# Performance work log

Hardware: AMD Instinct MI355X
Metric: run time of the kernel (lower is better)

The kernel has to match this reference:

```python
import jax, jax.numpy as jnp
import numpy as np

B, N = 2, 1024
DIM = 1024
DQK = 128
NUM_KEYS = 256
NUM_MEM = NUM_KEYS * NUM_KEYS
TOPK = 32
RANK = 2
HEADS = 2
DV = 512
KCONV = 5
MARGIN = 0.15
AUX_W = 0.1
MEM_LR = 10.0
RMS_EPS = 1.1920929e-07  # torch.finfo(float32).eps (RMSNorm eps=None default)
LN_EPS = 1e-5


def setup_inputs() -> dict:
    key = jax.random.key(0)
    ks = jax.random.split(key, 6)
    return {
        "tokens": jax.random.normal(ks[0], (B, N, DIM), jnp.float32),
        "rms_w": jnp.ones((DIM,), jnp.float32),
        "conv_w": jax.random.normal(ks[1], (DIM, 1, KCONV), jnp.float32) * 0.1,
        "conv_b": jnp.zeros((DIM,), jnp.float32),
        "wq": jax.random.normal(ks[2], (DQK, DIM), jnp.float32) * 0.02,
        "qln_w": jnp.ones((DQK,), jnp.float32),
        "keys": jax.random.normal(ks[3], (2, RANK, NUM_KEYS, DQK), jnp.float32) * 0.01,
        "core": jax.random.normal(ks[4], (HEADS, RANK, RANK), jnp.float32) * 0.01,
        "memories": jax.random.normal(ks[5], (NUM_MEM, DV), jnp.float32) * 0.01,
    }


def _forward(tokens, rms_w, conv_w, conv_b, wq, qln_w, keys, core, memories):
    # prenorm RMSNorm
    x = tokens * jax.lax.rsqrt(jnp.mean(tokens * tokens, -1, keepdims=True) + RMS_EPS) * rms_w
    # SVD of core; rank-1 merge vectors (first left/right singular vectors)
    u, s, vh = jnp.linalg.svd(core, full_matrices=False)
    u_vec = u[..., :, 0]   # (H, R)
    t_vec = vh[..., 0, :]  # (H, R)  == v[..., :, 0]
    aux = jnp.sum(jnp.mean(jnp.square(jax.nn.relu(s[:, 1:] - MARGIN)), -1)) * AUX_W
    # causal depthwise conv (left-pad KCONV-1)
    xc = jnp.swapaxes(x, 1, 2)  # (B, D, N)
    xc = jax.lax.conv_general_dilated(
        xc, conv_w, (1,), [(KCONV - 1, 0)],
        feature_group_count=DIM, dimension_numbers=('NCH', 'OIH', 'NCH'))
    x = jnp.swapaxes(xc + conv_b[None, :, None], 1, 2)
    # queries + LayerNorm (no bias). NOTE: original applies key_ln but then uses
    # the raw self.keys in the einsum, so key normalization is a no-op; replicated.
    q = x @ wq.T
    mu = jnp.mean(q, -1, keepdims=True)
    var = jnp.mean(jnp.square(q - mu), -1, keepdims=True)
    q = (q - mu) * jax.lax.rsqrt(var + LN_EPS) * qln_w
    # product-key scores: (2, B, N, M, R)
    sc = jnp.einsum('bnd,crmd->cbnmr', q, keys)
    row_sc, col_sc = sc[0], sc[1]  # (B, N, M, R)
    m_row = jnp.einsum('bnmr,hr->hbnm', row_sc, u_vec)
    m_col = jnp.einsum('bnmr,hr->hbnm', col_sc, t_vec)
    _, top_row = jax.lax.top_k(m_row, TOPK)  # (H, B, N, K)
    _, top_col = jax.lax.top_k(m_col, TOPK)
    # candidate flat memory indices: outer sum -> (H, B, N, K*K)
    idx = (top_row * NUM_KEYS)[..., :, None] + top_col[..., None, :]
    idx = idx.reshape(HEADS, B, N, TOPK * TOPK)
    # gather per-rank scores at the top row/col keys
    rs = jnp.broadcast_to(row_sc[None], (HEADS,) + row_sc.shape)
    cs = jnp.broadcast_to(col_sc[None], (HEADS,) + col_sc.shape)
    ri = jnp.broadcast_to(top_row[..., None], top_row.shape + (RANK,))
    ci = jnp.broadcast_to(top_col[..., None], top_col.shape + (RANK,))
    f_row = jnp.take_along_axis(rs, ri, axis=3)  # (H, B, N, K, R)
    f_col = jnp.take_along_axis(cs, ci, axis=3)
    # bilinear core combine over ranks -> (H, B, N, K, K)
    scores = jnp.einsum('hbnir,hbnjs,hrs->hbnij', f_row, f_col, core)
    scores = scores.reshape(HEADS, B, N, TOPK * TOPK)
    fs, top_m = jax.lax.top_k(scores, TOPK)
    f_idx = jnp.take_along_axis(idx, top_m, axis=-1)  # (H, B, N, K)
    fs = jax.nn.sigmoid(fs)
    # gather from memory table: (H, B, N, K, DV)
    mem = memories[f_idx]
    # scale_gradient exactly as written: detach(t) - s*t + detach(s*t)  (grad = -s)
    scaled = mem * MEM_LR
    mem = jax.lax.stop_gradient(mem) - scaled + jax.lax.stop_gradient(scaled)
    agg = jnp.einsum('hbnkd,hbnk->hbnd', mem, fs)
    out = jnp.transpose(agg, (1, 2, 0, 3)).reshape(B, N, HEADS * DV)
    # combine_values_to_out is Identity (heads * dim_values == dim)
    return out, aux


def reference(tokens, rms_w, conv_w, conv_b, wq, qln_w, keys, core, memories):
    return _forward(tokens, rms_w, conv_w, conv_b, wq, qln_w, keys, core, memories)
```

## Files before the change

### kernel.cpp

```cpp
#include <hip/hip_runtime.h>
#include <math.h>


#define ROWS 2048

__device__ inline double dsgn(double x, double y) { return (y >= 0.0) ? fabs(x) : -fabs(x); }

__device__ void dlasv2_dev(double f, double g, double h,
                           double& ssmin, double& ssmax,
                           double& snr, double& csr, double& snl, double& csl)
{
  const double EPSD = 2.2204460492503131e-16;
  double ft = f, fa = fabs(f), ht = h, ha = fabs(h);
  int pmax = 1;
  bool swp = (ha > fa);
  if (swp) { pmax = 3; double tp = ft; ft = ht; ht = tp; tp = fa; fa = ha; ha = tp; }
  double gt = g, ga = fabs(gt);
  double clt = 0.0, crt = 0.0, slt = 0.0, srt = 0.0;
  if (ga == 0.0) {
    ssmin = ha; ssmax = fa; clt = 1.0; crt = 1.0; slt = 0.0; srt = 0.0;
  } else {
    bool gasmal = true;
    if (ga > fa) {
      pmax = 2;
      if ((fa / ga) < EPSD) {
        gasmal = false;
        ssmax = ga;
        if (ha > 1.0) ssmin = fa / (ga / ha); else ssmin = (fa / ga) * ha;
        clt = 1.0; slt = ht / gt; srt = 1.0; crt = ft / gt;
      }
    }
    if (gasmal) {
      double dd = fa - ha, l;
      if (dd == fa) l = 1.0; else l = dd / fa;
      double m  = gt / ft;
      double t  = 2.0 - l;
      double mm = m * m, tt = t * t;
      double s  = sqrt(tt + mm);
      double r  = (l == 0.0) ? fabs(m) : sqrt(l * l + mm);
      double a  = 0.5 * (s + r);
      ssmin = ha / a;
      ssmax = fa * a;
      if (mm == 0.0) {
        if (l == 0.0) t = dsgn(2.0, ft) * dsgn(1.0, gt);
        else          t = gt / dsgn(dd, ft) + m / t;
      } else {
        t = (m / (s + t) + m / (r + l)) * (1.0 + a);
      }
      double ll = sqrt(t * t + 4.0);
      crt = 2.0 / ll;
      srt = t / ll;
      clt = (crt + srt * m) / a;
      slt = (ht / ft) * srt / a;
    }
  }
  if (swp) { csl = srt; snl = crt; csr = slt; snr = clt; }
  else     { csl = clt; snl = slt; csr = crt; snr = srt; }
  double tsign = 1.0;
  if (pmax == 1) tsign = dsgn(1.0, csr) * dsgn(1.0, csl) * dsgn(1.0, f);
  if (pmax == 2) tsign = dsgn(1.0, snr) * dsgn(1.0, csl) * dsgn(1.0, g);
  if (pmax == 3) tsign = dsgn(1.0, snr) * dsgn(1.0, snl) * dsgn(1.0, h);
  ssmax = dsgn(ssmax, tsign);
  ssmin = dsgn(ssmin, tsign * dsgn(1.0, f) * dsgn(1.0, h));
}

__global__ void svd_kernel(const float* __restrict__ core, float* __restrict__ misc,
                           float* __restrict__ aux_out)
{
  if (threadIdx.x != 0 || blockIdx.x != 0) return;
  double aux = 0.0;
  for (int hh = 0; hh < 2; hh++) {
    double a = (double)core[hh * 4 + 0];
    double b = (double)core[hh * 4 + 1];
    double c = (double)core[hh * 4 + 2];
    double d = (double)core[hh * 4 + 3];
    double tau = 0.0, v2 = 0.0, d1, e, d2;
    if (c != 0.0) {
      double nrm  = sqrt(a * a + c * c);
      double beta = (a >= 0.0) ? -nrm : nrm;
      tau = (beta - a) / beta;
      v2  = c / (a - beta);
      double wsum = b + v2 * d;
      d1 = beta;
      e  = b - tau * wsum;
      d2 = d - tau * v2 * wsum;
    } else { d1 = a; e = b; d2 = d; }
    double ssmin, ssmax, snr, csr, snl, csl;
    dlasv2_dev(d1, e, d2, ssmin, ssmax, snr, csr, snl, csl);
    double t0 = csl + v2 * snl;
    double u0 = csl - tau * t0;
    double u1 = snl - tau * v2 * t0;
    double sg = (ssmax < 0.0) ? -1.0 : 1.0;
    misc[hh * 2 + 0]     = (float)u0;
    misc[hh * 2 + 1]     = (float)u1;
    misc[4 + hh * 2 + 0] = (float)(sg * csr);
    misc[4 + hh * 2 + 1] = (float)(sg * snr);
    double s2 = fabs(ssmin);
    double rl = s2 - 0.15; if (rl < 0.0) rl = 0.0;
    aux += rl * rl;
  }
  aux_out[0] = (float)(aux * 0.1);
}

__global__ __launch_bounds__(256) void conv_kernel(const float* __restrict__ tokens,
                                                   const float* __restrict__ rms_w,
                                                   const float* __restrict__ conv_w,
                                                   const float* __restrict__ conv_b,
                                                   float* __restrict__ x2)
{
  __shared__ float x_l[12][1024];
  __shared__ float red[12][4];
  __shared__ float inv_s[12];
  const int t    = threadIdx.x;
  const int row0 = blockIdx.x * 8;
  const int n0   = row0 & 1023;
  const int c0   = t * 4;

  float sq[12];
  #pragma unroll
  for (int s = 0; s < 12; s++) {
    float4 v = make_float4(0.f, 0.f, 0.f, 0.f);
    if (n0 - 4 + s >= 0)
      v = *(const float4*)(tokens + (size_t)(row0 - 4 + s) * 1024 + c0);
    *(float4*)&x_l[s][c0] = v;
    sq[s] = v.x * v.x + v.y * v.y + v.z * v.z + v.w * v.w;
  }
  #pragma unroll
  for (int off = 32; off; off >>= 1) {
    #pragma unroll
    for (int s = 0; s < 12; s++) sq[s] += __shfl_down(sq[s], off, 64);
  }
  const int lane = t & 63, wv_id = t >> 6;
  if (lane == 0) {
    #pragma unroll
    for (int s = 0; s < 12; s++) red[s][wv_id] = sq[s];
  }
  __syncthreads();
  if (t < 12)
    inv_s[t] = rsqrtf((red[t][0] + red[t][1] + red[t][2] + red[t][3]) * (1.0f / 1024.0f)
                      + 1.1920929e-07f);
  __syncthreads();
  #pragma unroll
  for (int s = 0; s < 12; s++) {
    float iv = inv_s[s];
    float4 v = *(float4*)&x_l[s][c0];
    v.x *= iv; v.y *= iv; v.z *= iv; v.w *= iv;
    *(float4*)&x_l[s][c0] = v;
  }
  float wv[20];
  const float* cw = conv_w + (size_t)c0 * 5;
  #pragma unroll
  for (int i = 0; i < 5; i++) {
    float4 u = *(const float4*)(cw + i * 4);
    wv[i * 4 + 0] = u.x; wv[i * 4 + 1] = u.y; wv[i * 4 + 2] = u.z; wv[i * 4 + 3] = u.w;
  }
  float4 rw = *(const float4*)(rms_w + c0);
  float4 cb = *(const float4*)(conv_b + c0);
  #pragma unroll
  for (int r = 0; r < 8; r++) {
    float4 acc = make_float4(0.f, 0.f, 0.f, 0.f);
    #pragma unroll
    for (int k = 0; k < 5; k++) {
      float4 x4 = *(const float4*)&x_l[r + k][c0];
      acc.x = fmaf(x4.x, wv[0 * 5 + k], acc.x);
      acc.y = fmaf(x4.y, wv[1 * 5 + k], acc.y);
      acc.z = fmaf(x4.z, wv[2 * 5 + k], acc.z);
      acc.w = fmaf(x4.w, wv[3 * 5 + k], acc.w);
    }
    acc.x = acc.x * rw.x + cb.x;
    acc.y = acc.y * rw.y + cb.y;
    acc.z = acc.z * rw.z + cb.z;
    acc.w = acc.w * rw.w + cb.w;
    *(float4*)(x2 + (size_t)(row0 + r) * 1024 + c0) = acc;
  }
}

__global__ __launch_bounds__(256) void gemm_kernel(const float* __restrict__ A, int lda,
                                                   const float* __restrict__ Bm, int ldb,
                                                   float* __restrict__ C, int ldc,
                                                   int koffy, int coffy, int poffy)
{
  __shared__ __align__(16) float a_lds[32 * 64];
  __shared__ __align__(16) float b_lds[32 * 128];
  const int t  = threadIdx.x;
  const int rb = blockIdx.x * 64;
  const int kb = blockIdx.y * koffy;
  const int cb = blockIdx.y * coffy;
  C += (size_t)blockIdx.y * (size_t)poffy;
  const int tx = t & 31, ty = t >> 5;
  const int c0 = tx * 4, r0 = ty * 8;
  float acc[8][4];
  #pragma unroll
  for (int i = 0; i < 8; i++)
    #pragma unroll
    for (int j = 0; j < 4; j++) acc[i][j] = 0.0f;

  const int ra = t & 63,  kqa = (t >> 6) * 8;
  const int ob = t >> 1,  kqb = (t & 1) * 16;

  for (int kt = 0; kt < 4; kt++) {
    const int k0 = kb + kt * 32;
    {
      const float* ap = A + (size_t)(rb + ra) * lda + k0 + kqa;
      float4 a0 = *(const float4*)(ap);
      float4 a1 = *(const float4*)(ap + 4);
      a_lds[(kqa + 0) * 64 + ra] = a0.x;
      a_lds[(kqa + 1) * 64 + ra] = a0.y;
      a_lds[(kqa + 2) * 64 + ra] = a0.z;
      a_lds[(kqa + 3) * 64 + ra] = a0.w;
      a_lds[(kqa + 4) * 64 + ra] = a1.x;
      a_lds[(kqa + 5) * 64 + ra] = a1.y;
      a_lds[(kqa + 6) * 64 + ra] = a1.z;
      a_lds[(kqa + 7) * 64 + ra] = a1.w;
    }
    {
      const float* bp = Bm + (size_t)(cb + ob) * ldb + k0 + kqb;
      float4 b0 = *(const float4*)(bp);
      float4 b1 = *(const float4*)(bp + 4);
      float4 b2 = *(const float4*)(bp + 8);
      float4 b3 = *(const float4*)(bp + 12);
      b_lds[(kqb +  0) * 128 + ob] = b0.x;
      b_lds[(kqb +  1) * 128 + ob] = b0.y;
      b_lds[(kqb +  2) * 128 + ob] = b0.z;
      b_lds[(kqb +  3) * 128 + ob] = b0.w;
      b_lds[(kqb +  4) * 128 + ob] = b1.x;
      b_lds[(kqb +  5) * 128 + ob] = b1.y;
      b_lds[(kqb +  6) * 128 + ob] = b1.z;
      b_lds[(kqb +  7) * 128 + ob] = b1.w;
      b_lds[(kqb +  8) * 128 + ob] = b2.x;
      b_lds[(kqb +  9) * 128 + ob] = b2.y;
      b_lds[(kqb + 10) * 128 + ob] = b2.z;
      b_lds[(kqb + 11) * 128 + ob] = b2.w;
      b_lds[(kqb + 12) * 128 + ob] = b3.x;
      b_lds[(kqb + 13) * 128 + ob] = b3.y;
      b_lds[(kqb + 14) * 128 + ob] = b3.z;
      b_lds[(kqb + 15) * 128 + ob] = b3.w;
    }
    __syncthreads();
    #pragma unroll
    for (int k = 0; k < 32; k++) {
      float4 av0 = *(const float4*)(a_lds + k * 64 + r0);
      float4 av1 = *(const float4*)(a_lds + k * 64 + r0 + 4);
      float4 bv  = *(const float4*)(b_lds + k * 128 + c0);
      float ar[8] = {av0.x, av0.y, av0.z, av0.w, av1.x, av1.y, av1.z, av1.w};
      float br[4] = {bv.x, bv.y, bv.z, bv.w};
      #pragma unroll
      for (int i = 0; i < 8; i++)
        #pragma unroll
        for (int j = 0; j < 4; j++)
          acc[i][j] = fmaf(ar[i], br[j], acc[i][j]);
    }
    __syncthreads();
  }
  #pragma unroll
  for (int i = 0; i < 8; i++) {
    float4 o4; o4.x = acc[i][0]; o4.y = acc[i][1]; o4.z = acc[i][2]; o4.w = acc[i][3];
    *(float4*)(C + (size_t)(rb + r0 + i) * ldc + cb + c0) = o4;
  }
}

__global__ __launch_bounds__(128) void ln_kernel(const float* __restrict__ qpart,
                                                 const float* __restrict__ qln_w,
                                                 float* __restrict__ q)
{
  const int row = blockIdx.x, o = threadIdx.x;
  float v = 0.0f;
  #pragma unroll
  for (int g = 0; g < 8; g++) v += qpart[(size_t)g * (ROWS * 128) + (size_t)row * 128 + o];
  __shared__ float red[2];
  float s = v;
  for (int off = 32; off; off >>= 1) s += __shfl_down(s, off, 64);
  if ((o & 63) == 0) red[o >> 6] = s;
  __syncthreads();
  float mu  = (red[0] + red[1]) * (1.0f / 128.0f);
  float dv  = v - mu;
  float s2  = dv * dv;
  for (int off = 32; off; off >>= 1) s2 += __shfl_down(s2, off, 64);
  __syncthreads();
  if ((o & 63) == 0) red[o >> 6] = s2;
  __syncthreads();
  float var = (red[0] + red[1]) * (1.0f / 128.0f);
  q[(size_t)row * 128 + o] = dv * rsqrtf(var + 1e-5f) * qln_w[o];
}

__device__ inline unsigned f2ord(float f) {
  unsigned u = __float_as_uint(f);
  return (u & 0x80000000u) ? ~u : (u | 0x80000000u);
}
__device__ inline int lpc(unsigned long long m) {
  return __builtin_amdgcn_mbcnt_hi((unsigned)(m >> 32),
         __builtin_amdgcn_mbcnt_lo((unsigned)m, 0));
}

__global__ __launch_bounds__(256) void tail_kernel(const float* __restrict__ sc,
                                                   const float* __restrict__ misc,
                                                   const float* __restrict__ core,
                                                   const float* __restrict__ memories,
                                                   float* __restrict__ out)
{
  __shared__ float s_row[512];
  __shared__ float s_col[512];
  __shared__ int   tkbuf[4][32];
  __shared__ float mvals[4][32];
  __shared__ int   mcand[4][32];
  __shared__ int   s_idx[64];
  __shared__ float s_w[64];

  const int row = blockIdx.x;
  const int tid = threadIdx.x;
  {
    float4 v4 = ((const float4*)(sc + (size_t)row * 1024))[tid];
    float e[4] = {v4.x, v4.y, v4.z, v4.w};
    #pragma unroll
    for (int q2 = 0; q2 < 4; q2++) {
      int j = tid * 4 + q2;
      int m = j & 255, r = j >> 8;
      if (r < 2) s_row[m * 2 + r]       = e[q2];
      else       s_col[m * 2 + (r - 2)] = e[q2];
    }
  }
  __syncthreads();

  const int w = tid >> 6, lane = tid & 63;

  {
    const int h = w >> 1, side = w & 1;
    const float v0 = misc[side * 4 + h * 2 + 0];
    const float v1 = misc[side * 4 + h * 2 + 1];
    const float* sb = side ? s_col : s_row;
    const int mb = lane * 4;
    unsigned kk[4];
    #pragma unroll
    for (int i = 0; i < 4; i++) {
      float v = sb[(mb + i) * 2] * v0 + sb[(mb + i) * 2 + 1] * v1;
      kk[i] = f2ord(v);
    }
    unsigned tau = 0u;
    #pragma unroll
    for (int b = 31; b >= 0; --b) {
      unsigned cand = tau | (1u << b);
      int cnt = 0;
      #pragma unroll
      for (int i = 0; i < 4; i++) cnt += __popcll(__ballot(kk[i] >= cand));
      if (cnt >= 32) tau = cand;
    }
    unsigned long long bG[4], bE[4];
    int cntG = 0, sbG = 0, sbE = 0;
    #pragma unroll
    for (int i = 0; i < 4; i++) {
      bG[i] = __ballot(kk[i] > tau);
      bE[i] = __ballot(kk[i] == tau);
      cntG += __popcll(bG[i]);
      sbG  += lpc(bG[i]);
      sbE  += lpc(bE[i]);
    }
    const int need = 32 - cntG;
    int runG = 0, runE = 0;
    #pragma unroll
    for (int i = 0; i < 4; i++) {
      if (kk[i] > tau)       { tkbuf[w][sbG + runG] = mb + i; runG++; }
      else if (kk[i] == tau) {
        int r = sbE + runE;
        if (r < need) tkbuf[w][cntG + r] = mb + i;
        runE++;
      }
    }
  }
  __syncthreads();

  {
    const int h = w >> 1, half = w & 1;
    const float c00 = core[h * 4 + 0], c01 = core[h * 4 + 1];
    const float c10 = core[h * 4 + 2], c11 = core[h * 4 + 3];
    const int i_glob = half * 16 + (lane >> 2);
    const int ri = tkbuf[h * 2 + 0][i_glob];
    const float fr0 = s_row[ri * 2], fr1 = s_row[ri * 2 + 1];
    const float a0 = fr0 * c00 + fr1 * c10;
    const float a1 = fr0 * c01 + fr1 * c11;
    const int j0 = (lane & 3) * 8;
    float sv[8];
    unsigned kk[8];
    #pragma unroll
    for (int t2 = 0; t2 < 8; t2++) {
      int cj = tkbuf[h * 2 + 1][j0 + t2];
      sv[t2] = a0 * s_col[cj * 2] + a1 * s_col[cj * 2 + 1];
      kk[t2] = f2ord(sv[t2]);
    }
    unsigned tau = 0u;
    #pragma unroll
    for (int b = 31; b >= 0; --b) {
      unsigned cand = tau | (1u << b);
      int cnt = 0;
      #pragma unroll
      for (int i = 0; i < 8; i++) cnt += __popcll(__ballot(kk[i] >= cand));
      if (cnt >= 32) tau = cand;
    }
    unsigned long long bG[8], bE[8];
    int cntG = 0, sbG = 0, sbE = 0;
    #pragma unroll
    for (int i = 0; i < 8; i++) {
      bG[i] = __ballot(kk[i] > tau);
      bE[i] = __ballot(kk[i] == tau);
      cntG += __popcll(bG[i]);
      sbG  += lpc(bG[i]);
      sbE  += lpc(bE[i]);
    }
    const int need = 32 - cntG;
    int runG = 0, runE = 0;
    #pragma unroll
    for (int i = 0; i < 8; i++) {
      int c = i_glob * 32 + j0 + i;
      if (kk[i] > tau) {
        mvals[w][sbG + runG] = sv[i]; mcand[w][sbG + runG] = c; runG++;
      } else if (kk[i] == tau) {
        int r = sbE + runE;
        if (r < need) { mvals[w][cntG + r] = sv[i]; mcand[w][cntG + r] = c; }
        runE++;
      }
    }
  }
  __syncthreads();

  if (w < 2) {
    const int h = w;
    const int half2 = lane >> 5, k = lane & 31;
    const float v = mvals[h * 2 + half2][k];
    const int   c = mcand[h * 2 + half2][k];
    int cnt = 0;
    #pragma unroll 8
    for (int j = 0; j < 64; j++) {
      float u = mvals[h * 2 + (j >> 5)][j & 31];
      int  uc = mcand[h * 2 + (j >> 5)][j & 31];
      cnt += (u > v || (u == v && uc < c)) ? 1 : 0;
    }
    if (cnt < 32) {
      int ii = c >> 5, jj = c & 31;
      s_idx[h * 32 + cnt] = tkbuf[h * 2][ii] * 256 + tkbuf[h * 2 + 1][jj];
      s_w[h * 32 + cnt]   = 1.0f / (1.0f + expf(-v));
    }
  }
  __syncthreads();

  const int h2 = tid >> 7;
  const int d4 = tid & 127;
  const float* mb = memories + d4 * 4;
  float ax = 0.f, ay = 0.f, az = 0.f, aw = 0.f;
  #pragma unroll
  for (int b = 0; b < 4; b++) {
    int   mi[8]; float wg[8]; float4 v[8];
    #pragma unroll
    for (int i = 0; i < 8; i++) {
      mi[i] = s_idx[h2 * 32 + b * 8 + i];
      wg[i] = s_w[h2 * 32 + b * 8 + i];
    }
    #pragma unroll
    for (int i = 0; i < 8; i++)
      v[i] = *(const float4*)(mb + (size_t)mi[i] * 512);
    #pragma unroll
    for (int i = 0; i < 8; i++) {
      ax = fmaf(wg[i], v[i].x, ax);
      ay = fmaf(wg[i], v[i].y, ay);
      az = fmaf(wg[i], v[i].z, az);
      aw = fmaf(wg[i], v[i].w, aw);
    }
  }
  float4 o4; o4.x = ax; o4.y = ay; o4.z = az; o4.w = aw;
  ((float4*)out)[(size_t)row * 256 + tid] = o4;
}

extern "C" void kernel_launch(void* const* d_in, const int* in_sizes, int n_in,
                              void* d_out, int out_size, void* d_ws, size_t ws_size,
                              hipStream_t stream) {
  const float* tokens = (const float*)d_in[0];
  const float* rms_w  = (const float*)d_in[1];
  const float* conv_w = (const float*)d_in[2];
  const float* conv_b = (const float*)d_in[3];
  const float* wq     = (const float*)d_in[4];
  const float* qln_w  = (const float*)d_in[5];
  const float* keys   = (const float*)d_in[6];
  const float* core   = (const float*)d_in[7];
  const float* mems   = (const float*)d_in[8];
  float* out = (float*)d_out;
  float* ws  = (float*)d_ws;

  float* misc   = ws;
  float* x2     = ws + 4096;
  float* qpart  = x2 + 2097152;
  float* q      = qpart + 2097152;
  float* sc     = x2;

  svd_kernel <<<1, 64, 0, stream>>>(core, misc, out + 2097152);
  conv_kernel<<<ROWS / 8, 256, 0, stream>>>(tokens, rms_w, conv_w, conv_b, x2);
  gemm_kernel<<<dim3(32, 8), 256, 0, stream>>>(x2, 1024, wq, 1024,
                                               qpart, 128, 128, 0, ROWS * 128);
  ln_kernel  <<<ROWS, 128, 0, stream>>>(qpart, qln_w, q);
  gemm_kernel<<<dim3(32, 8), 256, 0, stream>>>(q, 128, keys, 128,
                                               sc, 1024, 0, 128, 0);
  tail_kernel<<<ROWS, 256, 0, stream>>>(sc, misc, core, mems, out);
}
```

Before: 279.7 us.

## Split tail into select and gather kernels, keep planar score layout in LDS

The fused tail kernel is split into a selection kernel, which writes the chosen memory indices and sigmoid weights to workspace, and a separate gather kernel that reads them and accumulates memory rows. The score row is now copied into shared memory as-is with one float4 store instead of being interleaved, and reads use vectorized planar accesses. Splitting lets the latency-bound selection and the bandwidth-bound gather each run without holding the other's resources. The cost is an extra launch and a small round-trip of indices and weights through global memory.

Result: slower. 286.2 us (+2.3%).

```diff
diff --git a/kernel.cpp b/kernel.cpp
--- a/kernel.cpp
+++ b/kernel.cpp
@@ -292,33 +292,20 @@
          __builtin_amdgcn_mbcnt_lo((unsigned)m, 0));
 }
 
-__global__ __launch_bounds__(256) void tail_kernel(const float* __restrict__ sc,
-                                                   const float* __restrict__ misc,
-                                                   const float* __restrict__ core,
-                                                   const float* __restrict__ memories,
-                                                   float* __restrict__ out)
-{
-  __shared__ float s_row[512];
-  __shared__ float s_col[512];
+__global__ __launch_bounds__(256) void select_kernel(const float* __restrict__ sc,
+                                                     const float* __restrict__ misc,
+                                                     const float* __restrict__ core,
+                                                     int*   __restrict__ sel_i,
+                                                     float* __restrict__ sel_w)
+{
+  __shared__ __align__(16) float s_pl[1024];
   __shared__ int   tkbuf[4][32];
   __shared__ float mvals[4][32];
   __shared__ int   mcand[4][32];
-  __shared__ int   s_idx[64];
-  __shared__ float s_w[64];
 
   const int row = blockIdx.x;
   const int tid = threadIdx.x;
-  {
-    float4 v4 = ((const float4*)(sc + (size_t)row * 1024))[tid];
-    float e[4] = {v4.x, v4.y, v4.z, v4.w};
-    #pragma unroll
-    for (int q2 = 0; q2 < 4; q2++) {
-      int j = tid * 4 + q2;
-      int m = j & 255, r = j >> 8;
-      if (r < 2) s_row[m * 2 + r]       = e[q2];
-      else       s_col[m * 2 + (r - 2)] = e[q2];
-    }
-  }
+  ((float4*)s_pl)[tid] = ((const float4*)(sc + (size_t)row * 1024))[tid];
   __syncthreads();
 
   const int w = tid >> 6, lane = tid & 63;
@@ -327,14 +314,16 @@
     const int h = w >> 1, side = w & 1;
     const float v0 = misc[side * 4 + h * 2 + 0];
     const float v1 = misc[side * 4 + h * 2 + 1];
-    const float* sb = side ? s_col : s_row;
+    const float* p0 = s_pl + side * 512;
+    const float* p1 = p0 + 256;
     const int mb = lane * 4;
+    float4 a4 = *(const float4*)(p0 + mb);
+    float4 b4 = *(const float4*)(p1 + mb);
     unsigned kk[4];
-    #pragma unroll
-    for (int i = 0; i < 4; i++) {
-      float v = sb[(mb + i) * 2] * v0 + sb[(mb + i) * 2 + 1] * v1;
-      kk[i] = f2ord(v);
-    }
+    kk[0] = f2ord(a4.x * v0 + b4.x * v1);
+    kk[1] = f2ord(a4.y * v0 + b4.y * v1);
+    kk[2] = f2ord(a4.z * v0 + b4.z * v1);
+    kk[3] = f2ord(a4.w * v0 + b4.w * v1);
     unsigned tau = 0u;
     #pragma unroll
     for (int b = 31; b >= 0; --b) {
@@ -374,7 +363,7 @@
     const float c10 = core[h * 4 + 2], c11 = core[h * 4 + 3];
     const int i_glob = half * 16 + (lane >> 2);
     const int ri = tkbuf[h * 2 + 0][i_glob];
-    const float fr0 = s_row[ri * 2], fr1 = s_row[ri * 2 + 1];
+    const float fr0 = s_pl[ri], fr1 = s_pl[256 + ri];
     const float a0 = fr0 * c00 + fr1 * c10;
     const float a1 = fr0 * c01 + fr1 * c11;
     const int j0 = (lane & 3) * 8;
@@ -383,7 +372,7 @@
     #pragma unroll
     for (int t2 = 0; t2 < 8; t2++) {
       int cj = tkbuf[h * 2 + 1][j0 + t2];
-      sv[t2] = a0 * s_col[cj * 2] + a1 * s_col[cj * 2 + 1];
+      sv[t2] = a0 * s_pl[512 + cj] + a1 * s_pl[768 + cj];
       kk[t2] = f2ord(sv[t2]);
     }
     unsigned tau = 0u;
@@ -435,12 +424,26 @@
     }
     if (cnt < 32) {
       int ii = c >> 5, jj = c & 31;
-      s_idx[h * 32 + cnt] = tkbuf[h * 2][ii] * 256 + tkbuf[h * 2 + 1][jj];
-      s_w[h * 32 + cnt]   = 1.0f / (1.0f + expf(-v));
-    }
-  }
-  __syncthreads();
-
+      sel_i[(size_t)row * 64 + h * 32 + cnt] = tkbuf[h * 2][ii] * 256 + tkbuf[h * 2 + 1][jj];
+      sel_w[(size_t)row * 64 + h * 32 + cnt] = 1.0f / (1.0f + expf(-v));
+    }
+  }
+}
+
+__global__ __launch_bounds__(256) void gather_kernel(const int*   __restrict__ sel_i,
+                                                     const float* __restrict__ sel_w,
+                                                     const float* __restrict__ memories,
+                                                     float* __restrict__ out)
+{
+  __shared__ int   s_idx[64];
+  __shared__ float s_w[64];
+  const int row = blockIdx.x;
+  const int tid = threadIdx.x;
+  if (tid < 64) {
+    s_idx[tid] = sel_i[(size_t)row * 64 + tid];
+    s_w[tid]   = sel_w[(size_t)row * 64 + tid];
+  }
+  __syncthreads();
   const int h2 = tid >> 7;
   const int d4 = tid & 127;
   const float* mb = memories + d4 * 4;
@@ -488,13 +491,16 @@
   float* qpart  = x2 + 2097152;
   float* q      = qpart + 2097152;
   float* sc     = x2;
-
-  svd_kernel <<<1, 64, 0, stream>>>(core, misc, out + 2097152);
-  conv_kernel<<<ROWS / 8, 256, 0, stream>>>(tokens, rms_w, conv_w, conv_b, x2);
-  gemm_kernel<<<dim3(32, 8), 256, 0, stream>>>(x2, 1024, wq, 1024,
-                                               qpart, 128, 128, 0, ROWS * 128);
-  ln_kernel  <<<ROWS, 128, 0, stream>>>(qpart, qln_w, q);
-  gemm_kernel<<<dim3(32, 8), 256, 0, stream>>>(q, 128, keys, 128,
-                                               sc, 1024, 0, 128, 0);
-  tail_kernel<<<ROWS, 256, 0, stream>>>(sc, misc, core, mems, out);
-}
+  int*   sel_i  = (int*)qpart;
+  float* sel_w  = qpart + 131072;
+
+  svd_kernel   <<<1, 64, 0, stream>>>(core, misc, out + 2097152);
+  conv_kernel  <<<ROWS / 8, 256, 0, stream>>>(tokens, rms_w, conv_w, conv_b, x2);
+  gemm_kernel  <<<dim3(32, 8), 256, 0, stream>>>(x2, 1024, wq, 1024,
+                                                 qpart, 128, 128, 0, ROWS * 128);
+  ln_kernel    <<<ROWS, 128, 0, stream>>>(qpart, qln_w, q);
+  gemm_kernel  <<<dim3(32, 8), 256, 0, stream>>>(q, 128, keys, 128,
+                                                 sc, 1024, 0, 128, 0);
+  select_kernel<<<ROWS, 256, 0, stream>>>(sc, misc, core, sel_i, sel_w);
+  gather_kernel<<<ROWS, 256, 0, stream>>>(sel_i, sel_w, mems, out);
+}
```
